# Performance work log

Hardware: AMD Instinct MI355X
Metric: run time of the kernel (lower is better)

Reference implementation:

```python
import jax, jax.numpy as jnp
import numpy as np

B, S, D, NH = 4, 2048, 1024, 16
HD = D // NH  # head dim = 64

def setup_inputs() -> dict:
    key = jax.random.key(0)
    ks = jax.random.split(key, 10)
    sc = 0.02
    return {
        "hidden_states": jax.random.normal(ks[0], (B, S, D), jnp.float32),
        "attention_mask": jnp.ones((B, S), jnp.float32),
        "Wq": jax.random.normal(ks[1], (D, D), jnp.float32) * sc,
        "bq": jnp.zeros((D,), jnp.float32),
        "Wk": jax.random.normal(ks[2], (D, D), jnp.float32) * sc,
        "bk": jnp.zeros((D,), jnp.float32),
        "Wv": jax.random.normal(ks[3], (D, D), jnp.float32) * sc,
        "bv": jnp.zeros((D,), jnp.float32),
        "Wo": jax.random.normal(ks[4], (D, D), jnp.float32) * sc,
        "bo": jnp.zeros((D,), jnp.float32),
    }

def reference(hidden_states, attention_mask, Wq, bq, Wk, bk, Wv, bv, Wo, bo):
    # projections: torch Linear computes x @ W.T + b
    q = hidden_states @ Wq.T + bq
    k = hidden_states @ Wk.T + bk
    v = hidden_states @ Wv.T + bv
    # [B,S,D] -> [B,NH,S,HD]
    def split_heads(x):
        return x.reshape(B, S, NH, HD).transpose(0, 2, 1, 3)
    q, k, v = split_heads(q), split_heads(k), split_heads(v)
    scores = jnp.einsum('bhqd,bhkd->bhqk', q, k) / jnp.sqrt(jnp.float32(HD))
    ext_mask = (1.0 - attention_mask)[:, None, None, :] * -10000.0
    scores = scores + ext_mask
    probs = jax.nn.softmax(scores, axis=-1)
    ctx = jnp.einsum('bhqk,bhkd->bhqd', probs, v)
    ctx = ctx.transpose(0, 2, 1, 3).reshape(B, S, D)
    return ctx @ Wo.T + bo
```

## Files before the change

kernel.cpp:

```cpp
#include <hip/hip_runtime.h>

typedef __attribute__((ext_vector_type(8))) short bf16x8;
typedef __attribute__((ext_vector_type(4))) float f32x4;

#define NBATCH 4
#define NSEQ   2048
#define NDIM   1024
#define NHEAD  16
#define HDIM   64
#define NM     (NBATCH*NSEQ)

static __device__ __forceinline__ unsigned short f2bf(float f) {
  unsigned u = __float_as_uint(f);
  u += 0x7fffu + ((u >> 16) & 1u);
  return (unsigned short)(u >> 16);
}

static __device__ __forceinline__ unsigned cvt_pk_bf16(float lo, float hi) {
  unsigned d;
  asm("v_cvt_pk_bf16_f32 %0, %1, %2" : "=v"(d) : "v"(lo), "v"(hi));
  return d;
}

static __device__ __forceinline__ void gload16(const void* g, void* l) {
  __builtin_amdgcn_global_load_lds(
      (const __attribute__((address_space(1))) unsigned*)g,
      (__attribute__((address_space(3))) unsigned*)l, 16, 0, 0);
}

__global__ __launch_bounds__(256) void cvt_kernel(
    const float* __restrict__ hs, const float* __restrict__ wq,
    const float* __restrict__ wk, const float* __restrict__ wv,
    const float* __restrict__ wo,
    unsigned short* __restrict__ hsb, unsigned short* __restrict__ wqb,
    unsigned short* __restrict__ wkb, unsigned short* __restrict__ wvb,
    unsigned short* __restrict__ wob) {
  long long t = (long long)blockIdx.x * blockDim.x + threadIdx.x;
  long long i4 = t * 4;
  const float* src; unsigned short* dst; long long base;
  if (i4 < 8388608LL) { src = hs; dst = hsb; base = i4; }
  else {
    long long j = i4 - 8388608LL;
    int w = (int)(j >> 20);
    base = j & 1048575LL;
    switch (w) { case 0: src=wq; dst=wqb; break; case 1: src=wk; dst=wkb; break;
                 case 2: src=wv; dst=wvb; break; default: src=wo; dst=wob; break; }
  }
  float4 v = *(const float4*)(src + base);
  unsigned short r0=f2bf(v.x), r1=f2bf(v.y), r2=f2bf(v.z), r3=f2bf(v.w);
  *(uint2*)(dst + base) = make_uint2((unsigned)r0 | ((unsigned)r1<<16),
                                     (unsigned)r2 | ((unsigned)r3<<16));
}

static __device__ __forceinline__ void gemm128(
    const unsigned short* __restrict__ A, const unsigned short* __restrict__ W,
    unsigned short* As, unsigned short* Bs, int m0, int n0, f32x4 (&acc)[4][4]) {
  const int tid = threadIdx.x;
  const int w = tid >> 6, l = tid & 63, g = l >> 4, r = l & 15;
  const int wm = w >> 1, wn = w & 1;
  const f32x4 z4 = {0.f, 0.f, 0.f, 0.f};
  #pragma unroll
  for (int i = 0; i < 4; ++i)
    #pragma unroll
    for (int j = 0; j < 4; ++j) acc[i][j] = z4;
  const int srow = (l >> 2);
  const int scol = (l & 3) * 8;
  for (int kt = 0; kt < 32; ++kt) {
    const int k0 = kt * 32;
    __syncthreads();
    #pragma unroll
    for (int i = 0; i < 2; ++i) {
      int c8 = w * 2 + i;
      int row = c8 * 16 + srow;
      gload16(A + (size_t)(m0 + row) * 1024 + k0 + scol, As + c8 * 512);
      gload16(W + (size_t)(n0 + row) * 1024 + k0 + scol, Bs + c8 * 512);
    }
    asm volatile("s_waitcnt vmcnt(0)" ::: "memory");
    __syncthreads();
    bf16x8 af[4], bf[4];
    #pragma unroll
    for (int ma = 0; ma < 4; ++ma)
      af[ma] = *(const bf16x8*)(As + (wm*64 + ma*16 + r) * 32 + g * 8);
    #pragma unroll
    for (int nb = 0; nb < 4; ++nb)
      bf[nb] = *(const bf16x8*)(Bs + (wn*64 + nb*16 + r) * 32 + g * 8);
    #pragma unroll
    for (int ma = 0; ma < 4; ++ma)
      #pragma unroll
      for (int nb = 0; nb < 4; ++nb)
        acc[ma][nb] = __builtin_amdgcn_mfma_f32_16x16x32_bf16(
            af[ma], bf[nb], acc[ma][nb], 0, 0, 0);
  }
}

__global__ __launch_bounds__(256) void qkv_gemm(
    const unsigned short* __restrict__ hsb,
    const unsigned short* __restrict__ wqb, const unsigned short* __restrict__ wkb,
    const unsigned short* __restrict__ wvb,
    const float* __restrict__ bq, const float* __restrict__ bk,
    const float* __restrict__ bv,
    unsigned short* __restrict__ qb, unsigned short* __restrict__ kb,
    unsigned short* __restrict__ vtb) {
  __shared__ unsigned short As[128*32], Bs[128*32];
  const int z = blockIdx.z;
  const unsigned short* W = (z == 0) ? wqb : (z == 1) ? wkb : wvb;
  const float* bias = (z == 0) ? bq : (z == 1) ? bk : bv;
  const int m0 = blockIdx.y * 128, n0 = blockIdx.x * 128;
  f32x4 acc[4][4];
  gemm128(hsb, W, As, Bs, m0, n0, acc);
  const int tid = threadIdx.x, w = tid >> 6, l = tid & 63, g = l >> 4, r = l & 15;
  const int wm = w >> 1, wn = w & 1;
  #pragma unroll
  for (int nb = 0; nb < 4; ++nb) {
    int n = n0 + wn*64 + nb*16 + r;
    float bval = bias[n];
    int h = n >> 6, d = n & 63;
    #pragma unroll
    for (int ma = 0; ma < 4; ++ma) {
      int mbase = m0 + wm*64 + ma*16 + g*4;
      if (z == 2) {
        int b = mbase >> 11, s0 = mbase & 2047;
        unsigned short u[4];
        #pragma unroll
        for (int j = 0; j < 4; ++j) u[j] = f2bf(acc[ma][nb][j] + bval);
        size_t idx = ((size_t)(b*16 + h) * 64 + d) * 2048 + s0;
        *(uint2*)(vtb + idx) = make_uint2((unsigned)u[0] | ((unsigned)u[1]<<16),
                                          (unsigned)u[2] | ((unsigned)u[3]<<16));
      } else {
        unsigned short* dst = (z == 0) ? qb : kb;
        float sc = (z == 0) ? 0.125f : 1.0f;
        #pragma unroll
        for (int j = 0; j < 4; ++j) {
          int m = mbase + j;
          int b = m >> 11, s = m & 2047;
          dst[((size_t)(b*16 + h) * 2048 + s) * 64 + d] = f2bf((acc[ma][nb][j] + bval) * sc);
        }
      }
    }
  }
}

__global__ __launch_bounds__(256) void flash_attn(
    const unsigned short* __restrict__ qb, const unsigned short* __restrict__ kb,
    const unsigned short* __restrict__ vtb, const float* __restrict__ mask,
    unsigned short* __restrict__ ctxb) {
  __shared__ unsigned short Kl[2][64*64], Vl[2][64*64], Pl[128*64];
  const int tid = threadIdx.x, w = tid >> 6, l = tid & 63, g = l >> 4, r = l & 15;
  const int bh = blockIdx.y, b = bh >> 4, h = bh & 15;
  const unsigned short* qh = qb  + (size_t)bh * 2048 * 64;
  const unsigned short* kh = kb  + (size_t)bh * 2048 * 64;
  const unsigned short* vh = vtb + (size_t)bh * 64 * 2048;
  const int q0 = blockIdx.x * 128;
  const int wq0 = q0 + w * 32;
  const float L2E = 1.44269504f;
  const float MC  = 14426.950408f;

  bf16x8 aq[2][2];
  #pragma unroll
  for (int mq = 0; mq < 2; ++mq)
    #pragma unroll
    for (int ks = 0; ks < 2; ++ks)
      aq[mq][ks] = *(const bf16x8*)(qh + (size_t)(wq0 + mq*16 + r) * 64 + ks*32 + g*8);

  const f32x4 z4 = {0.f, 0.f, 0.f, 0.f};
  f32x4 c[2][4];
  f32x4 cl[2];
  #pragma unroll
  for (int mq = 0; mq < 2; ++mq) {
    #pragma unroll
    for (int fn = 0; fn < 4; ++fn) c[mq][fn] = z4;
    cl[mq] = z4;
  }
  bf16x8 ones;
  #pragma unroll
  for (int i = 0; i < 8; ++i) ones[i] = (short)0x3F80;

  const int strow = (l >> 3);
  const int stsl  = l & 7;

  #pragma unroll
  for (int i = 0; i < 2; ++i) {
    int c8 = w * 2 + i;
    int row = c8 * 8 + strow;
    int sl = stsl ^ (row & 7);
    gload16(kh + (size_t)row * 64 + sl * 8, &Kl[0][c8 * 512]);
    gload16(vh + (size_t)row * 2048 + sl * 8, &Vl[0][c8 * 512]);
  }
  float mk[4];
  #pragma unroll
  for (int nk = 0; nk < 4; ++nk) mk[nk] = mask[b * 2048 + nk*16 + r];
  asm volatile("s_waitcnt vmcnt(0)" ::: "memory");
  __syncthreads();

  for (int kt = 0; kt < 32; ++kt) {
    const int cur = kt & 1;
    const int k0 = kt * 64;
    const unsigned short* Kc = Kl[cur];
    const unsigned short* Vc = Vl[cur];

    float mn[4];
    if (kt < 31) {
      unsigned short* Kn = Kl[cur ^ 1];
      unsigned short* Vn = Vl[cur ^ 1];
      #pragma unroll
      for (int i = 0; i < 2; ++i) {
        int c8 = w * 2 + i;
        int row = c8 * 8 + strow;
        int sl = stsl ^ (row & 7);
        gload16(kh + (size_t)(k0 + 64 + row) * 64 + sl * 8, Kn + c8 * 512);
        gload16(vh + (size_t)row * 2048 + k0 + 64 + sl * 8, Vn + c8 * 512);
      }
      #pragma unroll
      for (int nk = 0; nk < 4; ++nk) mn[nk] = mask[b * 2048 + k0 + 64 + nk*16 + r];
    }

    float madd2[4];
    #pragma unroll
    for (int nk = 0; nk < 4; ++nk) madd2[nk] = fmaf(mk[nk], MC, -MC);

    f32x4 sa[2][4];
    #pragma unroll
    for (int mq = 0; mq < 2; ++mq)
      #pragma unroll
      for (int nk = 0; nk < 4; ++nk) sa[mq][nk] = z4;
    #pragma unroll
    for (int nk = 0; nk < 4; ++nk) {
      int key = nk*16 + r;
      #pragma unroll
      for (int ks = 0; ks < 2; ++ks) {
        bf16x8 kf = *(const bf16x8*)(Kc + key*64 + (((ks*4 + g) ^ (key & 7)) * 8));
        sa[0][nk] = __builtin_amdgcn_mfma_f32_16x16x32_bf16(aq[0][ks], kf, sa[0][nk], 0,0,0);
        sa[1][nk] = __builtin_amdgcn_mfma_f32_16x16x32_bf16(aq[1][ks], kf, sa[1][nk], 0,0,0);
      }
    }

    #pragma unroll
    for (int mq = 0; mq < 2; ++mq) {
      #pragma unroll
      for (int j = 0; j < 4; ++j) {
        float p0 = exp2f(fmaf(sa[mq][0][j], L2E, madd2[0]));
        float p1 = exp2f(fmaf(sa[mq][1][j], L2E, madd2[1]));
        float p2 = exp2f(fmaf(sa[mq][2][j], L2E, madd2[2]));
        float p3 = exp2f(fmaf(sa[mq][3][j], L2E, madd2[3]));
        unsigned pk01 = cvt_pk_bf16(p0, p1);
        unsigned pk23 = cvt_pk_bf16(p2, p3);
        int row = w*32 + mq*16 + g*4 + j;
        unsigned short* rp = Pl + row*64;
        int rw = row & 7, rh = r >> 3, rb = r & 7;
        rp[((0 + rh) ^ rw)*8 + rb] = (unsigned short)pk01;
        rp[((2 + rh) ^ rw)*8 + rb] = (unsigned short)(pk01 >> 16);
        rp[((4 + rh) ^ rw)*8 + rb] = (unsigned short)pk23;
        rp[((6 + rh) ^ rw)*8 + rb] = (unsigned short)(pk23 >> 16);
      }
    }

    #pragma unroll
    for (int ks = 0; ks < 2; ++ks) {
      bf16x8 pa[2];
      #pragma unroll
      for (int fm = 0; fm < 2; ++fm) {
        int prow = w*32 + fm*16 + r;
        pa[fm] = *(const bf16x8*)(Pl + prow*64 + (((ks*4 + g) ^ (prow & 7)) * 8));
      }
      #pragma unroll
      for (int fn = 0; fn < 4; ++fn) {
        int vrow = fn*16 + r;
        bf16x8 vf = *(const bf16x8*)(Vc + vrow*64 + (((ks*4 + g) ^ (vrow & 7)) * 8));
        c[0][fn] = __builtin_amdgcn_mfma_f32_16x16x32_bf16(pa[0], vf, c[0][fn], 0,0,0);
        c[1][fn] = __builtin_amdgcn_mfma_f32_16x16x32_bf16(pa[1], vf, c[1][fn], 0,0,0);
      }
      cl[0] = __builtin_amdgcn_mfma_f32_16x16x32_bf16(pa[0], ones, cl[0], 0,0,0);
      cl[1] = __builtin_amdgcn_mfma_f32_16x16x32_bf16(pa[1], ones, cl[1], 0,0,0);
    }

    if (kt < 31) {
      #pragma unroll
      for (int nk = 0; nk < 4; ++nk) mk[nk] = mn[nk];
    }
    asm volatile("s_waitcnt vmcnt(0)" ::: "memory");
    __syncthreads();
  }

  #pragma unroll
  for (int mq = 0; mq < 2; ++mq)
    #pragma unroll
    for (int j = 0; j < 4; ++j) {
      float inv = 1.0f / cl[mq][j];
      int srow = q0 + w*32 + mq*16 + g*4 + j;
      size_t base = ((size_t)(b * 2048 + srow)) * 1024 + h * 64;
      #pragma unroll
      for (int fn = 0; fn < 4; ++fn)
        ctxb[base + fn*16 + r] = f2bf(c[mq][fn][j] * inv);
    }
}

__global__ __launch_bounds__(256) void out_gemm(
    const unsigned short* __restrict__ ctxb, const unsigned short* __restrict__ wob,
    const float* __restrict__ bo, float* __restrict__ out) {
  __shared__ unsigned short As[128*32], Bs[128*32];
  const int m0 = blockIdx.y * 128, n0 = blockIdx.x * 128;
  f32x4 acc[4][4];
  gemm128(ctxb, wob, As, Bs, m0, n0, acc);
  const int tid = threadIdx.x, w = tid >> 6, l = tid & 63, g = l >> 4, r = l & 15;
  const int wm = w >> 1, wn = w & 1;
  #pragma unroll
  for (int nb = 0; nb < 4; ++nb) {
    int n = n0 + wn*64 + nb*16 + r;
    float bval = bo[n];
    #pragma unroll
    for (int ma = 0; ma < 4; ++ma)
      #pragma unroll
      for (int j = 0; j < 4; ++j) {
        int m = m0 + wm*64 + ma*16 + g*4 + j;
        out[(size_t)m * 1024 + n] = acc[ma][nb][j] + bval;
      }
  }
}

extern "C" void kernel_launch(void* const* d_in, const int* in_sizes, int n_in,
                              void* d_out, int out_size, void* d_ws, size_t ws_size,
                              hipStream_t stream) {
  const float* hs   = (const float*)d_in[0];
  const float* mask = (const float*)d_in[1];
  const float* wq   = (const float*)d_in[2];
  const float* bq   = (const float*)d_in[3];
  const float* wk   = (const float*)d_in[4];
  const float* bk   = (const float*)d_in[5];
  const float* wv   = (const float*)d_in[6];
  const float* bv   = (const float*)d_in[7];
  const float* wo   = (const float*)d_in[8];
  const float* bo   = (const float*)d_in[9];
  float* out = (float*)d_out;
  char* ws = (char*)d_ws;
  unsigned short* hsb = (unsigned short*)(ws);
  unsigned short* wqb = (unsigned short*)(ws + (16ull << 20));
  unsigned short* wkb = (unsigned short*)(ws + (18ull << 20));
  unsigned short* wvb = (unsigned short*)(ws + (20ull << 20));
  unsigned short* wob = (unsigned short*)(ws + (22ull << 20));
  unsigned short* qb  = (unsigned short*)(ws + (24ull << 20));
  unsigned short* kb  = (unsigned short*)(ws + (40ull << 20));
  unsigned short* vtb = (unsigned short*)(ws + (56ull << 20));
  unsigned short* ctb = (unsigned short*)(ws + (72ull << 20));

  cvt_kernel<<<12288, 256, 0, stream>>>(hs, wq, wk, wv, wo, hsb, wqb, wkb, wvb, wob);
  qkv_gemm<<<dim3(8, 64, 3), 256, 0, stream>>>(hsb, wqb, wkb, wvb, bq, bk, bv, qb, kb, vtb);
  flash_attn<<<dim3(16, 64), 256, 0, stream>>>(qb, kb, vtb, mask, ctb);
  out_gemm<<<dim3(8, 64), 256, 0, stream>>>(ctb, wob, bo, out);
}
```

Before: 385.9 us.

## Keep attention probabilities in registers via transposed MFMA and permlane swaps

The flash attention kernel now computes S^T by swapping the MFMA operand order, so each lane holds scores for one query row across keys. The bf16 probabilities are rearranged into the PV MFMA operand layout with permlane32/permlane16 swaps instead of being written to and read back from an LDS P buffer. This removes the P shared-memory round trip and frees LDS, which could raise occupancy. The mask is now loaded per tile as float4 instead of being prefetched, and the context output is stored as 8-byte vectors. It relies on gfx950 permlane swap builtins and on the lane mapping being correct.

```diff
diff --git a/kernel.cpp b/kernel.cpp
--- a/kernel.cpp
+++ b/kernel.cpp
@@ -2,13 +2,14 @@
 
 typedef __attribute__((ext_vector_type(8))) short bf16x8;
 typedef __attribute__((ext_vector_type(4))) float f32x4;
+typedef __attribute__((ext_vector_type(2))) unsigned u32x2;
+typedef __attribute__((ext_vector_type(4))) unsigned u32x4;
 
 #define NBATCH 4
 #define NSEQ   2048
 #define NDIM   1024
 #define NHEAD  16
 #define HDIM   64
-#define NM     (NBATCH*NSEQ)
 
 static __device__ __forceinline__ unsigned short f2bf(float f) {
   unsigned u = __float_as_uint(f);
@@ -141,15 +142,15 @@
 }
 
 __global__ __launch_bounds__(256) void flash_attn(
-    const unsigned short* __restrict__ qb, const unsigned short* __restrict__ kb,
-    const unsigned short* __restrict__ vtb, const float* __restrict__ mask,
+    const unsigned short* __restrict__ qg, const unsigned short* __restrict__ kg,
+    const unsigned short* __restrict__ vg, const float* __restrict__ mask,
     unsigned short* __restrict__ ctxb) {
-  __shared__ unsigned short Kl[2][64*64], Vl[2][64*64], Pl[128*64];
+  __shared__ unsigned short Kl[2][4096], Vl[2][4096];
   const int tid = threadIdx.x, w = tid >> 6, l = tid & 63, g = l >> 4, r = l & 15;
   const int bh = blockIdx.y, b = bh >> 4, h = bh & 15;
-  const unsigned short* qh = qb  + (size_t)bh * 2048 * 64;
-  const unsigned short* kh = kb  + (size_t)bh * 2048 * 64;
-  const unsigned short* vh = vtb + (size_t)bh * 64 * 2048;
+  const unsigned short* qh = qg + (size_t)bh * 2048 * 64;
+  const unsigned short* kh = kg + (size_t)bh * 2048 * 64;
+  const unsigned short* vh = vg + (size_t)bh * 64 * 2048;
   const int q0 = blockIdx.x * 128;
   const int wq0 = q0 + w * 32;
   const float L2E = 1.44269504f;
@@ -175,7 +176,7 @@
   #pragma unroll
   for (int i = 0; i < 8; ++i) ones[i] = (short)0x3F80;
 
-  const int strow = (l >> 3);
+  const int strow = l >> 3;
   const int stsl  = l & 7;
 
   #pragma unroll
@@ -186,9 +187,6 @@
     gload16(kh + (size_t)row * 64 + sl * 8, &Kl[0][c8 * 512]);
     gload16(vh + (size_t)row * 2048 + sl * 8, &Vl[0][c8 * 512]);
   }
-  float mk[4];
-  #pragma unroll
-  for (int nk = 0; nk < 4; ++nk) mk[nk] = mask[b * 2048 + nk*16 + r];
   asm volatile("s_waitcnt vmcnt(0)" ::: "memory");
   __syncthreads();
 
@@ -198,7 +196,6 @@
     const unsigned short* Kc = Kl[cur];
     const unsigned short* Vc = Vl[cur];
 
-    float mn[4];
     if (kt < 31) {
       unsigned short* Kn = Kl[cur ^ 1];
       unsigned short* Vn = Vl[cur ^ 1];
@@ -210,88 +207,94 @@
         gload16(kh + (size_t)(k0 + 64 + row) * 64 + sl * 8, Kn + c8 * 512);
         gload16(vh + (size_t)row * 2048 + k0 + 64 + sl * 8, Vn + c8 * 512);
       }
-      #pragma unroll
-      for (int nk = 0; nk < 4; ++nk) mn[nk] = mask[b * 2048 + k0 + 64 + nk*16 + r];
-    }
-
-    float madd2[4];
-    #pragma unroll
-    for (int nk = 0; nk < 4; ++nk) madd2[nk] = fmaf(mk[nk], MC, -MC);
+    }
+
+    float md[16];
+    #pragma unroll
+    for (int kq = 0; kq < 4; ++kq) {
+      float4 m4 = *(const float4*)(mask + b * 2048 + k0 + kq*16 + g*4);
+      md[kq*4+0] = fmaf(m4.x, MC, -MC);
+      md[kq*4+1] = fmaf(m4.y, MC, -MC);
+      md[kq*4+2] = fmaf(m4.z, MC, -MC);
+      md[kq*4+3] = fmaf(m4.w, MC, -MC);
+    }
 
     f32x4 sa[2][4];
     #pragma unroll
     for (int mq = 0; mq < 2; ++mq)
       #pragma unroll
-      for (int nk = 0; nk < 4; ++nk) sa[mq][nk] = z4;
-    #pragma unroll
-    for (int nk = 0; nk < 4; ++nk) {
-      int key = nk*16 + r;
+      for (int kq = 0; kq < 4; ++kq) sa[mq][kq] = z4;
+    #pragma unroll
+    for (int kq = 0; kq < 4; ++kq) {
+      int key = kq*16 + r;
       #pragma unroll
       for (int ks = 0; ks < 2; ++ks) {
         bf16x8 kf = *(const bf16x8*)(Kc + key*64 + (((ks*4 + g) ^ (key & 7)) * 8));
-        sa[0][nk] = __builtin_amdgcn_mfma_f32_16x16x32_bf16(aq[0][ks], kf, sa[0][nk], 0,0,0);
-        sa[1][nk] = __builtin_amdgcn_mfma_f32_16x16x32_bf16(aq[1][ks], kf, sa[1][nk], 0,0,0);
-      }
-    }
-
+        sa[0][kq] = __builtin_amdgcn_mfma_f32_16x16x32_bf16(kf, aq[0][ks], sa[0][kq], 0,0,0);
+        sa[1][kq] = __builtin_amdgcn_mfma_f32_16x16x32_bf16(kf, aq[1][ks], sa[1][kq], 0,0,0);
+      }
+    }
+
+    bf16x8 pb[2][2];
     #pragma unroll
     for (int mq = 0; mq < 2; ++mq) {
-      #pragma unroll
-      for (int j = 0; j < 4; ++j) {
-        float p0 = exp2f(fmaf(sa[mq][0][j], L2E, madd2[0]));
-        float p1 = exp2f(fmaf(sa[mq][1][j], L2E, madd2[1]));
-        float p2 = exp2f(fmaf(sa[mq][2][j], L2E, madd2[2]));
-        float p3 = exp2f(fmaf(sa[mq][3][j], L2E, madd2[3]));
-        unsigned pk01 = cvt_pk_bf16(p0, p1);
-        unsigned pk23 = cvt_pk_bf16(p2, p3);
-        int row = w*32 + mq*16 + g*4 + j;
-        unsigned short* rp = Pl + row*64;
-        int rw = row & 7, rh = r >> 3, rb = r & 7;
-        rp[((0 + rh) ^ rw)*8 + rb] = (unsigned short)pk01;
-        rp[((2 + rh) ^ rw)*8 + rb] = (unsigned short)(pk01 >> 16);
-        rp[((4 + rh) ^ rw)*8 + rb] = (unsigned short)pk23;
-        rp[((6 + rh) ^ rw)*8 + rb] = (unsigned short)(pk23 >> 16);
+      unsigned pk[4][2];
+      #pragma unroll
+      for (int kq = 0; kq < 4; ++kq) {
+        float p0 = exp2f(fmaf(sa[mq][kq][0], L2E, md[kq*4+0]));
+        float p1 = exp2f(fmaf(sa[mq][kq][1], L2E, md[kq*4+1]));
+        float p2 = exp2f(fmaf(sa[mq][kq][2], L2E, md[kq*4+2]));
+        float p3 = exp2f(fmaf(sa[mq][kq][3], L2E, md[kq*4+3]));
+        pk[kq][0] = cvt_pk_bf16(p0, p1);
+        pk[kq][1] = cvt_pk_bf16(p2, p3);
+      }
+      #pragma unroll
+      for (int ch = 0; ch < 2; ++ch) {
+        u32x4 fr;
+        #pragma unroll
+        for (int i = 0; i < 2; ++i) {
+          u32x2 s1 = __builtin_amdgcn_permlane32_swap(pk[ch*2][i], pk[ch*2+1][i], false, false);
+          u32x2 s2 = __builtin_amdgcn_permlane16_swap(s1.x, s1.y, false, false);
+          fr[i]     = s2.x;
+          fr[2 + i] = s2.y;
+        }
+        pb[mq][ch] = __builtin_bit_cast(bf16x8, fr);
       }
     }
 
     #pragma unroll
     for (int ks = 0; ks < 2; ++ks) {
-      bf16x8 pa[2];
-      #pragma unroll
-      for (int fm = 0; fm < 2; ++fm) {
-        int prow = w*32 + fm*16 + r;
-        pa[fm] = *(const bf16x8*)(Pl + prow*64 + (((ks*4 + g) ^ (prow & 7)) * 8));
-      }
       #pragma unroll
       for (int fn = 0; fn < 4; ++fn) {
         int vrow = fn*16 + r;
         bf16x8 vf = *(const bf16x8*)(Vc + vrow*64 + (((ks*4 + g) ^ (vrow & 7)) * 8));
-        c[0][fn] = __builtin_amdgcn_mfma_f32_16x16x32_bf16(pa[0], vf, c[0][fn], 0,0,0);
-        c[1][fn] = __builtin_amdgcn_mfma_f32_16x16x32_bf16(pa[1], vf, c[1][fn], 0,0,0);
-      }
-      cl[0] = __builtin_amdgcn_mfma_f32_16x16x32_bf16(pa[0], ones, cl[0], 0,0,0);
-      cl[1] = __builtin_amdgcn_mfma_f32_16x16x32_bf16(pa[1], ones, cl[1], 0,0,0);
-    }
-
-    if (kt < 31) {
-      #pragma unroll
-      for (int nk = 0; nk < 4; ++nk) mk[nk] = mn[nk];
-    }
+        c[0][fn] = __builtin_amdgcn_mfma_f32_16x16x32_bf16(vf, pb[0][ks], c[0][fn], 0,0,0);
+        c[1][fn] = __builtin_amdgcn_mfma_f32_16x16x32_bf16(vf, pb[1][ks], c[1][fn], 0,0,0);
+      }
+      cl[0] = __builtin_amdgcn_mfma_f32_16x16x32_bf16(ones, pb[0][ks], cl[0], 0,0,0);
+      cl[1] = __builtin_amdgcn_mfma_f32_16x16x32_bf16(ones, pb[1][ks], cl[1], 0,0,0);
+    }
+
     asm volatile("s_waitcnt vmcnt(0)" ::: "memory");
     __syncthreads();
   }
 
   #pragma unroll
-  for (int mq = 0; mq < 2; ++mq)
-    #pragma unroll
-    for (int j = 0; j < 4; ++j) {
-      float inv = 1.0f / cl[mq][j];
-      int srow = q0 + w*32 + mq*16 + g*4 + j;
-      size_t base = ((size_t)(b * 2048 + srow)) * 1024 + h * 64;
-      #pragma unroll
-      for (int fn = 0; fn < 4; ++fn)
-        ctxb[base + fn*16 + r] = f2bf(c[mq][fn][j] * inv);
-    }
+  for (int mq = 0; mq < 2; ++mq) {
+    float inv = 1.0f / cl[mq][0];
+    int srow = q0 + w*32 + mq*16 + r;
+    size_t base = ((size_t)(b * 2048 + srow)) * 1024 + h * 64;
+    #pragma unroll
+    for (int fn = 0; fn < 4; ++fn) {
+      unsigned short u0 = f2bf(c[mq][fn][0] * inv);
+      unsigned short u1 = f2bf(c[mq][fn][1] * inv);
+      unsigned short u2 = f2bf(c[mq][fn][2] * inv);
+      unsigned short u3 = f2bf(c[mq][fn][3] * inv);
+      *(uint2*)(ctxb + base + fn*16 + g*4) =
+          make_uint2((unsigned)u0 | ((unsigned)u1<<16),
+                     (unsigned)u2 | ((unsigned)u3<<16));
+    }
+  }
 }
 
 __global__ __launch_bounds__(256) void out_gemm(
```

Result: faster. 350.7 us (-9.1%).
